# Optimization experiments

Measured on AMD Instinct MI355X. Metric: run time of the kernel, lower is better.

The kernel has to match this reference:

```python
import jax, jax.numpy as jnp
import numpy as np

# The torch module expresses conv as unfold -> linear (no bias) -> fold(1x1).
# That pipeline is mathematically exactly a VALID cross-correlation with the
# Linear weight reshaped to OIHW (torch unfold flattens patches in (C, kh, kw)
# order, matching Linear's in_features layout). We implement it as the
# efficient direct conv, which computes identical math.

B = 2048

def setup_inputs() -> dict:
    key = jax.random.key(0)
    k1, k2, k3 = jax.random.split(key, 3)
    x = jax.random.normal(k1, (B, 784), dtype=jnp.float32)
    # nn.Linear(49 -> 10, bias=False) and nn.Linear(250 -> 10, bias=False)
    W1 = jax.random.normal(k2, (10, 49), dtype=jnp.float32) * (1.0 / np.sqrt(49.0))
    W2 = jax.random.normal(k3, (10, 250), dtype=jnp.float32) * (1.0 / np.sqrt(250.0))
    return {"x": x, "W1": W1, "W2": W2}

def _conv(x, w_oihw):
    return jax.lax.conv_general_dilated(
        x, w_oihw, window_strides=(1, 1), padding='VALID',
        dimension_numbers=('NCHW', 'OIHW', 'NCHW'))

def _relu_ratio(x_base):
    # x = relu(x_base); ratio = x / x_base with NaN/Inf -> 0 (matches
    # calculate_ratio: 0/0 -> NaN -> 0, relu(neg)/neg -> -0 -> stays 0)
    x = jax.nn.relu(x_base)
    rat = x / x_base
    rat = jnp.where(jnp.isnan(rat) | jnp.isinf(rat), jnp.float32(0.0), rat)
    return x, rat

def reference(x, W1, W2):
    b = x.shape[0]
    h = x.reshape(b, 1, 28, 28)
    # layer 1: unfold(7x7) + linear(49->10) + fold == conv, out (b,10,22,22)
    h = _conv(h, W1.reshape(10, 1, 7, 7))
    h, rat1 = _relu_ratio(h)
    # layer 2: unfold(5x5) + linear(250->10) + fold == conv, out (b,10,18,18)
    h = _conv(h, W2.reshape(10, 10, 5, 5))
    h, rat2 = _relu_ratio(h)
    return (h, rat1, rat2)
```

## Files before the change

kernel.cpp:

```cpp
#include <hip/hip_runtime.h>


#define THREADS 256

__global__ __launch_bounds__(THREADS, 4) void brewcnn_fused(
    const float* __restrict__ x,
    const float* __restrict__ Wa,
    const float* __restrict__ Wb,
    float* __restrict__ out,
    int nimg)
{
    __shared__ __align__(16) float s_x[28 * 28];
    __shared__ __align__(16) float s_h[10][22 * 24];
    __shared__ __align__(16) float s_wa[490];
    __shared__ __align__(16) float s_wb[2500];

    const int img = blockIdx.x;
    const int tid = threadIdx.x;

    if (tid < 196)
        reinterpret_cast<float4*>(s_x)[tid] =
            reinterpret_cast<const float4*>(x + img * 784)[tid];
    if (tid < 122)
        reinterpret_cast<float4*>(s_wa)[tid] =
            reinterpret_cast<const float4*>(Wa)[tid];
    if (tid < 2) s_wa[488 + tid] = Wa[488 + tid];
    for (int i = tid; i < 625; i += THREADS)
        reinterpret_cast<float4*>(s_wb)[i] =
            reinterpret_cast<const float4*>(Wb)[i];
    __syncthreads();

    const int h2_base = img * 3240;
    const int r1_base = nimg * 3240 + img * 4840;
    const int r2_base = nimg * 8080 + img * 3240;

    if (tid < 220) {
        const int row = tid / 10;
        const int oc  = tid - row * 10;
        float acc[22];
#pragma unroll
        for (int i = 0; i < 22; ++i) acc[i] = 0.0f;

        const float* wrow = s_wa + oc * 49;
        for (int ky = 0; ky < 7; ++ky) {
            float in[28];
            const float4* rp = reinterpret_cast<const float4*>(s_x + (row + ky) * 28);
#pragma unroll
            for (int j = 0; j < 7; ++j) {
                float4 v = rp[j];
                in[4*j] = v.x; in[4*j+1] = v.y; in[4*j+2] = v.z; in[4*j+3] = v.w;
            }
            float w[7];
#pragma unroll
            for (int k = 0; k < 7; ++k) w[k] = wrow[ky * 7 + k];
#pragma unroll
            for (int kx = 0; kx < 7; ++kx)
#pragma unroll
                for (int px = 0; px < 22; ++px)
                    acc[px] = fmaf(in[px + kx], w[kx], acc[px]);
        }

        float r1v[22];
#pragma unroll
        for (int px = 0; px < 22; ++px) {
            const float h = acc[px];
            acc[px] = h > 0.0f ? h : 0.0f;
            r1v[px] = h > 0.0f ? 1.0f : 0.0f;
        }
        float* hdst = &s_h[oc][row * 24];
#pragma unroll
        for (int j = 0; j < 5; ++j)
            reinterpret_cast<float4*>(hdst)[j] =
                make_float4(acc[4*j], acc[4*j+1], acc[4*j+2], acc[4*j+3]);
        hdst[20] = acc[20];
        hdst[21] = acc[21];

        float* r1p = out + r1_base + oc * 484 + row * 22;
#pragma unroll
        for (int j = 0; j < 11; ++j)
            reinterpret_cast<float2*>(r1p)[j] = make_float2(r1v[2*j], r1v[2*j+1]);
    }
    __syncthreads();

    if (tid < 180) {
        const int row = tid / 10;
        const int oc  = tid - row * 10;
        float acc[18];
#pragma unroll
        for (int i = 0; i < 18; ++i) acc[i] = 0.0f;

        const float* wbase = s_wb + oc * 250;
#pragma unroll 1
        for (int ic = 0; ic < 10; ++ic) {
            const float* hbase = &s_h[ic][0];
            const float* wic = wbase + ic * 25;
            for (int ky = 0; ky < 5; ++ky) {
                float in[24];
                const float4* rp = reinterpret_cast<const float4*>(hbase + (row + ky) * 24);
#pragma unroll
                for (int j = 0; j < 6; ++j) {
                    float4 v = rp[j];
                    in[4*j] = v.x; in[4*j+1] = v.y; in[4*j+2] = v.z; in[4*j+3] = v.w;
                }
                float w[5];
#pragma unroll
                for (int k = 0; k < 5; ++k) w[k] = wic[ky * 5 + k];
#pragma unroll
                for (int kx = 0; kx < 5; ++kx)
#pragma unroll
                    for (int px = 0; px < 18; ++px)
                        acc[px] = fmaf(in[px + kx], w[kx], acc[px]);
            }
        }

        float hv[18], rv[18];
#pragma unroll
        for (int px = 0; px < 18; ++px) {
            const float h = acc[px];
            hv[px] = h > 0.0f ? h : 0.0f;
            rv[px] = h > 0.0f ? 1.0f : 0.0f;
        }
        float* h2p = out + h2_base + oc * 324 + row * 18;
        float* r2p = out + r2_base + oc * 324 + row * 18;
#pragma unroll
        for (int j = 0; j < 9; ++j) {
            reinterpret_cast<float2*>(h2p)[j] = make_float2(hv[2*j], hv[2*j+1]);
            reinterpret_cast<float2*>(r2p)[j] = make_float2(rv[2*j], rv[2*j+1]);
        }
    }
}

extern "C" void kernel_launch(void* const* d_in, const int* in_sizes, int n_in,
                              void* d_out, int out_size, void* d_ws, size_t ws_size,
                              hipStream_t stream) {
    const float* x  = (const float*)d_in[0];
    const float* Wa = (const float*)d_in[1];
    const float* Wb = (const float*)d_in[2];
    float* out = (float*)d_out;
    const int nimg = in_sizes[0] / 784;

    brewcnn_fused<<<nimg, THREADS, 0, stream>>>(x, Wa, Wb, out, nimg);
}
```

Before: 161.7 us.

## Split fused CNN kernel into two conv kernels with workspace intermediate and register tiling

```diff
diff --git a/kernel.cpp b/kernel.cpp
--- a/kernel.cpp
+++ b/kernel.cpp
@@ -1,14 +1,142 @@
 #include <hip/hip_runtime.h>
 
 
-#define THREADS 256
-
-__global__ __launch_bounds__(THREADS, 4) void brewcnn_fused(
+#define TA 128
+#define TB 128
+
+__global__ __launch_bounds__(TA, 4) void brew_conv1(
     const float* __restrict__ x,
     const float* __restrict__ Wa,
+    float* __restrict__ out,
+    float* __restrict__ h1,
+    int nimg)
+{
+    __shared__ __align__(16) float s_x[784];
+    const int img = blockIdx.x;
+    const int tid = threadIdx.x;
+
+    {
+        const float4* xin = reinterpret_cast<const float4*>(x + img * 784);
+        float4* sx = reinterpret_cast<float4*>(s_x);
+        for (int i = tid; i < 196; i += TA) sx[i] = xin[i];
+    }
+    __syncthreads();
+
+    const int t   = tid < 110 ? tid : 109;
+    const int row = t / 5;
+    const int g   = t - row * 5;
+    const int c   = (g < 4) ? 5 * g : 17;
+
+    float acc[10][5];
+#pragma unroll
+    for (int oc = 0; oc < 10; ++oc)
+#pragma unroll
+        for (int k = 0; k < 5; ++k) acc[oc][k] = 0.0f;
+
+#pragma unroll 1
+    for (int ky = 0; ky < 7; ++ky) {
+        float in[11];
+        const float* rp = s_x + (row + ky) * 28 + c;
+#pragma unroll
+        for (int j = 0; j < 11; ++j) in[j] = rp[j];
+
+#pragma unroll
+        for (int oc = 0; oc < 10; ++oc) {
+            const float* wp = Wa + oc * 49 + ky * 7;
+#pragma unroll
+            for (int kx = 0; kx < 7; ++kx) {
+                const float w = wp[kx];
+#pragma unroll
+                for (int k = 0; k < 5; ++k)
+                    acc[oc][k] = fmaf(in[k + kx], w, acc[oc][k]);
+            }
+        }
+    }
+
+    const int r1_base = nimg * 3240 + img * 4840;
+    float* hb = h1 + img * 5280;
+#pragma unroll
+    for (int oc = 0; oc < 10; ++oc) {
+        float* hp = hb + oc * 528 + row * 24 + c;
+        float* rp = out + r1_base + oc * 484 + row * 22 + c;
+#pragma unroll
+        for (int k = 0; k < 5; ++k) {
+            const float h = acc[oc][k];
+            hp[k] = h > 0.0f ? h : 0.0f;
+            rp[k] = h > 0.0f ? 1.0f : 0.0f;
+        }
+    }
+}
+
+__global__ __launch_bounds__(TB, 4) void brew_conv2(
+    const float* __restrict__ h1,
     const float* __restrict__ Wb,
     float* __restrict__ out,
     int nimg)
+{
+    __shared__ __align__(16) float s_h[10 * 528];
+    const int img = blockIdx.x;
+    const int tid = threadIdx.x;
+
+    {
+        const float4* src = reinterpret_cast<const float4*>(h1 + img * 5280);
+        float4* dst = reinterpret_cast<float4*>(s_h);
+        for (int i = tid; i < 1320; i += TB) dst[i] = src[i];
+    }
+    __syncthreads();
+
+    const int t   = tid < 108 ? tid : 107;
+    const int row = t / 6;
+    const int c   = 3 * (t - row * 6);
+
+    float acc[10][3];
+#pragma unroll
+    for (int oc = 0; oc < 10; ++oc)
+#pragma unroll
+        for (int k = 0; k < 3; ++k) acc[oc][k] = 0.0f;
+
+#pragma unroll 1
+    for (int ic = 0; ic < 10; ++ic) {
+        const float* hb = s_h + ic * 528 + row * 24 + c;
+#pragma unroll
+        for (int ky = 0; ky < 5; ++ky) {
+            float in[7];
+            const float* rp = hb + ky * 24;
+#pragma unroll
+            for (int j = 0; j < 7; ++j) in[j] = rp[j];
+
+#pragma unroll
+            for (int oc = 0; oc < 10; ++oc) {
+                const float* wp = Wb + oc * 250 + ic * 25 + ky * 5;
+#pragma unroll
+                for (int kx = 0; kx < 5; ++kx) {
+                    const float w = wp[kx];
+#pragma unroll
+                    for (int k = 0; k < 3; ++k)
+                        acc[oc][k] = fmaf(in[k + kx], w, acc[oc][k]);
+                }
+            }
+        }
+    }
+
+    const int h2_base = img * 3240;
+    const int r2_base = nimg * 8080 + img * 3240;
+#pragma unroll
+    for (int oc = 0; oc < 10; ++oc) {
+        float* h2p = out + h2_base + oc * 324 + row * 18 + c;
+        float* r2p = out + r2_base + oc * 324 + row * 18 + c;
+#pragma unroll
+        for (int k = 0; k < 3; ++k) {
+            const float h = acc[oc][k];
+            h2p[k] = h > 0.0f ? h : 0.0f;
+            r2p[k] = h > 0.0f ? 1.0f : 0.0f;
+        }
+    }
+}
+
+__global__ __launch_bounds__(256, 4) void brewcnn_fused_fb(
+    const float* __restrict__ x, const float* __restrict__ Wa,
+    const float* __restrict__ Wb, float* __restrict__ out, int nimg)
 {
     __shared__ __align__(16) float s_x[28 * 28];
     __shared__ __align__(16) float s_h[10][22 * 24];
@@ -25,9 +153,8 @@
         reinterpret_cast<float4*>(s_wa)[tid] =
             reinterpret_cast<const float4*>(Wa)[tid];
     if (tid < 2) s_wa[488 + tid] = Wa[488 + tid];
-    for (int i = tid; i < 625; i += THREADS)
-        reinterpret_cast<float4*>(s_wb)[i] =
-            reinterpret_cast<const float4*>(Wb)[i];
+    for (int i = tid; i < 625; i += 256)
+        reinterpret_cast<float4*>(s_wb)[i] = reinterpret_cast<const float4*>(Wb)[i];
     __syncthreads();
 
     const int h2_base = img * 3240;
@@ -35,12 +162,10 @@
     const int r2_base = nimg * 8080 + img * 3240;
 
     if (tid < 220) {
-        const int row = tid / 10;
-        const int oc  = tid - row * 10;
+        const int row = tid / 10, oc = tid - row * 10;
         float acc[22];
 #pragma unroll
         for (int i = 0; i < 22; ++i) acc[i] = 0.0f;
-
         const float* wrow = s_wa + oc * 49;
         for (int ky = 0; ky < 7; ++ky) {
             float in[28];
@@ -59,7 +184,6 @@
                 for (int px = 0; px < 22; ++px)
                     acc[px] = fmaf(in[px + kx], w[kx], acc[px]);
         }
-
         float r1v[22];
 #pragma unroll
         for (int px = 0; px < 22; ++px) {
@@ -72,9 +196,7 @@
         for (int j = 0; j < 5; ++j)
             reinterpret_cast<float4*>(hdst)[j] =
                 make_float4(acc[4*j], acc[4*j+1], acc[4*j+2], acc[4*j+3]);
-        hdst[20] = acc[20];
-        hdst[21] = acc[21];
-
+        hdst[20] = acc[20]; hdst[21] = acc[21];
         float* r1p = out + r1_base + oc * 484 + row * 22;
 #pragma unroll
         for (int j = 0; j < 11; ++j)
@@ -83,12 +205,10 @@
     __syncthreads();
 
     if (tid < 180) {
-        const int row = tid / 10;
-        const int oc  = tid - row * 10;
+        const int row = tid / 10, oc = tid - row * 10;
         float acc[18];
 #pragma unroll
         for (int i = 0; i < 18; ++i) acc[i] = 0.0f;
-
         const float* wbase = s_wb + oc * 250;
 #pragma unroll 1
         for (int ic = 0; ic < 10; ++ic) {
@@ -112,7 +232,6 @@
                         acc[px] = fmaf(in[px + kx], w[kx], acc[px]);
             }
         }
-
         float hv[18], rv[18];
 #pragma unroll
         for (int px = 0; px < 18; ++px) {
@@ -139,5 +258,12 @@
     float* out = (float*)d_out;
     const int nimg = in_sizes[0] / 784;
 
-    brewcnn_fused<<<nimg, THREADS, 0, stream>>>(x, Wa, Wb, out, nimg);
-}
+    const size_t h1_bytes = (size_t)nimg * 5280 * sizeof(float);
+    if (ws_size >= h1_bytes) {
+        float* h1 = (float*)d_ws;
+        brew_conv1<<<nimg, TA, 0, stream>>>(x, Wa, out, h1, nimg);
+        brew_conv2<<<nimg, TB, 0, stream>>>(h1, Wb, out, nimg);
+    } else {
+        brewcnn_fused_fb<<<nimg, 256, 0, stream>>>(x, Wa, Wb, out, nimg);
+    }
+}
```

New measurement: 250.3 us. 1.55x slower.
